# Performance work log

Hardware: AMD Instinct MI355X
Metric: run time of the kernel (lower is better)

## Reference

```python
import jax, jax.numpy as jnp
import numpy as np

N_NODES = 50000


def gcn_layer(x, src, dst, ew, W, b, n_nodes):
    # PyG GCNConv: add self-loops (weight 1), symmetric deg^-1/2 normalization,
    # linear transform, scatter-add aggregation at destination, then bias.
    loop = jnp.arange(n_nodes, dtype=src.dtype)
    s = jnp.concatenate([src, loop])
    d = jnp.concatenate([dst, loop])
    w = jnp.concatenate([ew, jnp.ones((n_nodes,), dtype=ew.dtype)])
    deg = jax.ops.segment_sum(w, d, num_segments=n_nodes)  # [N]
    dinv = jnp.where(deg > 0, jax.lax.rsqrt(jnp.where(deg > 0, deg, 1.0)), 0.0)
    norm = dinv[s] * w * dinv[d]  # [E+N]
    h = x @ W  # [N, out]
    msg = h[s] * norm[:, None]  # gather + scale, [E+N, out]
    out = jax.ops.segment_sum(msg, d, num_segments=n_nodes)  # scatter-add
    return out + b


def setup_inputs() -> dict:
    key = jax.random.key(0)
    k1, k2, k3, k4, k5, k6, k7 = jax.random.split(key, 7)
    N, E, C_IN, C_OUT = N_NODES, 600000, 128, 128
    x = jax.random.normal(k1, (N, C_IN), dtype=jnp.float32)
    edge_index = jax.random.randint(k2, (2, E), 0, N, dtype=jnp.int64)
    edge_weight = jax.random.uniform(k3, (E,), dtype=jnp.float32)
    # Glorot-style init like PyG's Linear default
    s1 = 1.0 / np.sqrt(C_IN)
    s2 = 1.0 / np.sqrt(C_OUT)
    W1 = jax.random.uniform(k4, (C_IN, C_OUT), jnp.float32, -s1, s1)
    b1 = jnp.zeros((C_OUT,), dtype=jnp.float32)
    W2 = jax.random.uniform(k5, (C_OUT, C_OUT), jnp.float32, -s2, s2)
    b2 = jnp.zeros((C_OUT,), dtype=jnp.float32)
    return {"x": x, "edge_index": edge_index, "edge_weight": edge_weight,
            "W1": W1, "b1": b1, "W2": W2, "b2": b2}


def reference(x, edge_index, edge_weight, W1, b1, W2, b2):
    src, dst = edge_index[0], edge_index[1]
    h = jax.nn.relu(gcn_layer(x, src, dst, edge_weight, W1, b1, N_NODES))
    return jax.nn.relu(gcn_layer(h, src, dst, edge_weight, W2, b2, N_NODES))
```

## Files before the change

### kernel.cpp

```cpp
#include <hip/hip_runtime.h>
#include <math.h>

#define CH   128
#define CH4  32
#define TPB  256
#define SCANB 1024
#define WIMG 16384
#define NREP 8
#define FIXS 1048576.0f

typedef __attribute__((ext_vector_type(8))) short short8;
typedef __attribute__((ext_vector_type(4))) float floatx4;
typedef __attribute__((ext_vector_type(8))) float float8;
typedef unsigned long long u64;

static __device__ __forceinline__ unsigned short f2bf(float f) {
    unsigned u = __float_as_uint(f);
    return (unsigned short)((u + 0x7fffu + ((u >> 16) & 1u)) >> 16);
}
static __device__ __forceinline__ float bf2f(unsigned short s) {
    return __uint_as_float(((unsigned)s) << 16);
}
static __device__ __forceinline__ float8 bf8_to_f8(short8 u) {
    float8 f;
    #pragma unroll
    for (int i = 0; i < 8; ++i) f[i] = bf2f((unsigned short)u[i]);
    return f;
}

__global__ void k_prep(const float* __restrict__ W1, const float* __restrict__ W2,
                       short* __restrict__ Wsplit, float4* __restrict__ zbase,
                       int nzero4, int nbPrep) {
    int bx = blockIdx.x;
    if (bx >= nbPrep) {
        int i = (bx - nbPrep) * TPB + threadIdx.x;
        if (i < nzero4) zbase[i] = make_float4(0.f, 0.f, 0.f, 0.f);
        return;
    }
    int i = bx * TPB + threadIdx.x;
    if (i >= 2 * CH * CH) return;
    int layer = i >> 14;
    int idx   = i & 16383;
    int k = idx >> 7, c = idx & 127;
    float w = (layer ? W2 : W1)[k * CH + c];
    unsigned short hi = f2bf(w);
    unsigned short lo = f2bf(w - bf2f(hi));
    int colh = c >> 6, nn = c & 63;
    int kt = k >> 5, q = (k & 31) >> 3, j = k & 7;
    int ns = nn >> 4, ln = q * 16 + (nn & 15);
    size_t base = (size_t)(layer * 2 + colh) * WIMG;
    size_t off  = ((size_t)(kt * 4 + ns) * 64 + ln) * 8 + j;
    Wsplit[base + off]        = (short)hi;
    Wsplit[base + 8192 + off] = (short)lo;
}

static __device__ __forceinline__ void gemm_body_f32(
        const float* __restrict__ X, const short* __restrict__ Wfrag,
        unsigned short* __restrict__ H, int n, int tile, int colh, int tid) {
    __shared__ __align__(16) short sW[2][4][4][64][8];
    {
        const float4* gsrc = (const float4*)Wfrag;
        float4* ldst = (float4*)sW;
        #pragma unroll
        for (int i = 0; i < 8; ++i)
            ldst[i * TPB + tid] = gsrc[i * TPB + tid];
    }
    __syncthreads();

    const int lane = tid & 63;
    const int wv   = tid >> 6;
    const int q    = lane >> 4;
    const int m    = lane & 15;
    const int row0 = tile * 64 + wv * 16;
    if (row0 >= n) return;

    int rrow = row0 + m;
    if (rrow > n - 1) rrow = n - 1;

    const float4* xr = (const float4*)(X + (size_t)rrow * CH);
    float4 xa[4][2];
    #pragma unroll
    for (int kt = 0; kt < 4; ++kt) {
        xa[kt][0] = xr[kt * 8 + q * 2 + 0];
        xa[kt][1] = xr[kt * 8 + q * 2 + 1];
    }

    floatx4 acc[4];
    #pragma unroll
    for (int ns = 0; ns < 4; ++ns) acc[ns] = (floatx4){0.f, 0.f, 0.f, 0.f};

    #pragma unroll
    for (int kt = 0; kt < 4; ++kt) {
        float xf[8] = { xa[kt][0].x, xa[kt][0].y, xa[kt][0].z, xa[kt][0].w,
                        xa[kt][1].x, xa[kt][1].y, xa[kt][1].z, xa[kt][1].w };
        short8 ah, al;
        #pragma unroll
        for (int j = 0; j < 8; ++j) {
            float v = xf[j];
            unsigned short h = f2bf(v);
            ah[j] = (short)h;
            al[j] = (short)f2bf(v - bf2f(h));
        }
        #pragma unroll
        for (int ns = 0; ns < 4; ++ns) {
            short8 bh = *(const short8*)&sW[0][kt][ns][lane][0];
            short8 bl = *(const short8*)&sW[1][kt][ns][lane][0];
            acc[ns] = __builtin_amdgcn_mfma_f32_16x16x32_bf16(ah, bh, acc[ns], 0, 0, 0);
            acc[ns] = __builtin_amdgcn_mfma_f32_16x16x32_bf16(al, bh, acc[ns], 0, 0, 0);
            acc[ns] = __builtin_amdgcn_mfma_f32_16x16x32_bf16(ah, bl, acc[ns], 0, 0, 0);
        }
    }

    #pragma unroll
    for (int ns = 0; ns < 4; ++ns) {
        #pragma unroll
        for (int reg = 0; reg < 4; ++reg) {
            int r = row0 + q * 4 + reg;
            if (r < n)
                H[(size_t)r * CH + colh * 64 + ns * 16 + m] = f2bf(acc[ns][reg]);
        }
    }
}

__global__ __launch_bounds__(TPB, 4)
void k_gemm_rank(const float* __restrict__ X, const short* __restrict__ Wsplit,
                 unsigned short* __restrict__ H, int n,
                 const int* __restrict__ dst, const float* __restrict__ ew,
                 u64* __restrict__ counts_rep, int E, int nbE4, int Np) {
    int bx = blockIdx.x;
    if (bx < nbE4) {
        int stride = nbE4 * TPB;
        int e = bx * TPB + threadIdx.x;
        #pragma unroll
        for (int it = 0; it < 4; ++it, e += stride) {
            if (e < E) {
                int d = dst[e];
                if ((unsigned)d < (unsigned)n) {
                    int rep = e & (NREP - 1);
                    u64 pk = (1ull << 40) |
                             (u64)(unsigned)__float2uint_rn(ew[e] * FIXS);
                    atomicAdd(&counts_rep[(size_t)rep * Np + d], pk);
                }
            }
        }
    } else {
        bx -= nbE4;
        int colh = bx & 1;
        gemm_body_f32(X, Wsplit + (size_t)colh * WIMG, H, n, bx >> 1, colh,
                      threadIdx.x);
    }
}

__global__ __launch_bounds__(SCANB)
void k_scan1(const u64* __restrict__ counts_rep, int Np,
             int* __restrict__ counts_tot, int* __restrict__ repoff8,
             int* __restrict__ row_start, float* __restrict__ dinv,
             int* __restrict__ partials, int* __restrict__ pp_s,
             int* __restrict__ done, int nb, int n) {
    __shared__ int swt[SCANB / 64];
    __shared__ int slastS;
    const int tid  = threadIdx.x;
    const int lane = tid & 63;
    const int wid  = tid >> 6;
    const int gid  = blockIdx.x * SCANB + tid;

    int c[NREP];
    int v = 0;
    u64 wsum = 0;
    #pragma unroll
    for (int r = 0; r < NREP; ++r) {
        u64 pk = (gid < n) ? counts_rep[(size_t)r * Np + gid] : 0ull;
        c[r] = (int)(pk >> 40);
        wsum += pk & ((1ull << 40) - 1);
        v += c[r];
    }
    int inc = v;
    #pragma unroll
    for (int off = 1; off < 64; off <<= 1) {
        int t = __shfl_up(inc, off, 64);
        if (lane >= off) inc += t;
    }
    if (lane == 63) swt[wid] = inc;
    __syncthreads();
    if (wid == 0) {
        int wv_ = (lane < SCANB / 64) ? swt[lane] : 0;
        int winc = wv_;
        #pragma unroll
        for (int off = 1; off < SCANB / 64; off <<= 1) {
            int t = __shfl_up(winc, off, 64);
            if (lane >= off) winc += t;
        }
        if (lane < SCANB / 64) swt[lane] = winc - wv_;
    }
    __syncthreads();
    const int myincl = inc + swt[wid];

    if (gid < n) {
        row_start[gid]  = myincl - v;
        counts_tot[gid] = v;
        dinv[gid] = rsqrtf(1.0f + (float)wsum * (1.0f / FIXS));
        int pre = 0;
        int ro[NREP];
        #pragma unroll
        for (int r = 0; r < NREP; ++r) { ro[r] = pre; pre += c[r]; }
        ((int4*)repoff8)[gid * 2 + 0] = make_int4(ro[0], ro[1], ro[2], ro[3]);
        ((int4*)repoff8)[gid * 2 + 1] = make_int4(ro[4], ro[5], ro[6], ro[7]);
    }
    if (tid == SCANB - 1) {
        partials[blockIdx.x] = myincl;
        __threadfence();
        int old = atomicAdd(done, 1);
        slastS = (old == nb - 1);
    }
    __syncthreads();
    if (slastS && tid < 64) {
        int pv = (tid < nb) ? atomicAdd(&partials[tid], 0) : 0;
        int i2 = pv;
        #pragma unroll
        for (int off = 1; off < 64; off <<= 1) {
            int t = __shfl_up(i2, off, 64);
            if ((tid & 63) >= off) i2 += t;
        }
        if (tid < nb) pp_s[tid] = i2 - pv;
    }
}

__global__ void k_fill(const int* __restrict__ src, const int* __restrict__ dst,
                       const float* __restrict__ ew, const int* __restrict__ row_start,
                       const int* __restrict__ pp_s, const int* __restrict__ repoff8,
                       u64* __restrict__ counts_rep, const float* __restrict__ dinv,
                       int2* __restrict__ edges, int E, int n, int Np) {
    int e = blockIdx.x * blockDim.x + threadIdx.x;
    if (e >= E) return;
    int s = src[e], d = dst[e];
    if ((unsigned)s >= (unsigned)n || (unsigned)d >= (unsigned)n) return;
    int rep = e & (NREP - 1);
    u64 old = atomicAdd(&counts_rep[(size_t)rep * Np + d], 0ull - (1ull << 40));
    int slot = (int)(old >> 40) - 1;
    int base = row_start[d] + pp_s[d >> 10] + repoff8[d * NREP + rep];
    edges[base + slot] = make_int2(s, __float_as_int(ew[e] * dinv[s]));
}

static __device__ __forceinline__ float8 agg_node8(
        const short8* __restrict__ h8, const int2* __restrict__ edges,
        float di, const float8 b, int node, int tx,
        const int* __restrict__ row_start, const int* __restrict__ pp_s,
        const int* __restrict__ counts) {
    float8 hv = bf8_to_f8(h8[(size_t)node * 16 + tx]);
    float8 acc;
    #pragma unroll
    for (int i = 0; i < 8; ++i) acc[i] = 0.f;

    int j   = row_start[node] + pp_s[node >> 10];
    int end = j + counts[node];

    for (; j + 8 <= end; j += 8) {
        int2 e[8];
        #pragma unroll
        for (int i = 0; i < 8; ++i) e[i] = edges[j + i];
        short8 g[8];
        #pragma unroll
        for (int i = 0; i < 8; ++i) g[i] = h8[(size_t)e[i].x * 16 + tx];
        #pragma unroll
        for (int i = 0; i < 8; ++i) {
            float w = __int_as_float(e[i].y);
            float8 gf = bf8_to_f8(g[i]);
            #pragma unroll
            for (int c = 0; c < 8; ++c) acc[c] += gf[c] * w;
        }
    }
    if (j + 4 <= end) {
        int2 e[4];
        #pragma unroll
        for (int i = 0; i < 4; ++i) e[i] = edges[j + i];
        short8 g[4];
        #pragma unroll
        for (int i = 0; i < 4; ++i) g[i] = h8[(size_t)e[i].x * 16 + tx];
        #pragma unroll
        for (int i = 0; i < 4; ++i) {
            float w = __int_as_float(e[i].y);
            float8 gf = bf8_to_f8(g[i]);
            #pragma unroll
            for (int c = 0; c < 8; ++c) acc[c] += gf[c] * w;
        }
        j += 4;
    }
    for (; j < end; ++j) {
        int2 e0 = edges[j];
        float w0 = __int_as_float(e0.y);
        float8 gf = bf8_to_f8(h8[(size_t)e0.x * 16 + tx]);
        #pragma unroll
        for (int c = 0; c < 8; ++c) acc[c] += gf[c] * w0;
    }

    float di2 = di * di;
    float8 o;
    #pragma unroll
    for (int c = 0; c < 8; ++c) o[c] = di2 * hv[c] + di * acc[c] + b[c];
    return o;
}

__global__ __launch_bounds__(TPB)
void k_agg_gemm(const unsigned short* __restrict__ h,
                const int* __restrict__ row_start, const int* __restrict__ pp_s,
                const int* __restrict__ counts, const int2* __restrict__ edges,
                const float* __restrict__ dinv, const float* __restrict__ bias,
                const short* __restrict__ W2img,
                unsigned short* __restrict__ h2, int n) {
    __shared__ __align__(16) short8 tile[16 * 17];
    const int tid = threadIdx.x;

    const int bnode0 = (int)blockIdx.x * 16;
    const int tx = tid & 15;
    const int tg = tid >> 4;
    const int node = bnode0 + tg;
    float8 b;
    #pragma unroll
    for (int c = 0; c < 8; ++c) b[c] = bias[tx * 8 + c];
    short8 u;
    if (node < n) {
        float8 o = agg_node8((const short8*)h, edges, dinv[node], b, node,
                             tx, row_start, pp_s, counts);
        #pragma unroll
        for (int c = 0; c < 8; ++c) u[c] = (short)f2bf(fmaxf(o[c], 0.f));
    } else {
        #pragma unroll
        for (int c = 0; c < 8; ++c) u[c] = 0;
    }
    tile[tg * 17 + tx] = u;
    __syncthreads();

    const int lane = tid & 63;
    const int wv   = tid >> 6;
    const int q    = lane >> 4;
    const int m    = lane & 15;
    const int ch   = wv & 1;
    const int ns0  = (wv >> 1) * 2;

    short8 a[4];
    #pragma unroll
    for (int kt = 0; kt < 4; ++kt)
        a[kt] = tile[m * 17 + kt * 4 + q];

    const short8* w2f = (const short8*)(W2img + (size_t)ch * WIMG);

    floatx4 acc[2];
    #pragma unroll
    for (int i = 0; i < 2; ++i) acc[i] = (floatx4){0.f, 0.f, 0.f, 0.f};

    #pragma unroll
    for (int kt = 0; kt < 4; ++kt) {
        #pragma unroll
        for (int i = 0; i < 2; ++i) {
            short8 bh = w2f[(kt * 4 + ns0 + i) * 64 + lane];
            acc[i] = __builtin_amdgcn_mfma_f32_16x16x32_bf16(a[kt], bh, acc[i],
                                                             0, 0, 0);
        }
    }

    #pragma unroll
    for (int i = 0; i < 2; ++i)
        #pragma unroll
        for (int reg = 0; reg < 4; ++reg) {
            int r = bnode0 + q * 4 + reg;
            if (r < n)
                h2[(size_t)r * CH + ch * 64 + (ns0 + i) * 16 + m] =
                    f2bf(acc[i][reg]);
        }
}

__global__ __launch_bounds__(TPB)
void k_aggregate2(const unsigned short* __restrict__ h,
                  const int* __restrict__ row_start, const int* __restrict__ pp_s,
                  const int* __restrict__ counts, const int2* __restrict__ edges,
                  const float* __restrict__ dinv, const float* __restrict__ bias,
                  float* __restrict__ out, int n) {
    int t = blockIdx.x * blockDim.x + threadIdx.x;
    int node = t >> 4;
    if (node >= n) return;
    int tx = t & 15;
    float8 b;
    #pragma unroll
    for (int c = 0; c < 8; ++c) b[c] = bias[tx * 8 + c];
    float8 o = agg_node8((const short8*)h, edges, dinv[node], b, node, tx,
                         row_start, pp_s, counts);
    float4 lo = make_float4(fmaxf(o[0], 0.f), fmaxf(o[1], 0.f),
                            fmaxf(o[2], 0.f), fmaxf(o[3], 0.f));
    float4 hi = make_float4(fmaxf(o[4], 0.f), fmaxf(o[5], 0.f),
                            fmaxf(o[6], 0.f), fmaxf(o[7], 0.f));
    ((float4*)out)[(size_t)node * CH4 + tx * 2 + 0] = lo;
    ((float4*)out)[(size_t)node * CH4 + tx * 2 + 1] = hi;
}

extern "C" void kernel_launch(void* const* d_in, const int* in_sizes, int n_in,
                              void* d_out, int out_size, void* d_ws, size_t ws_size,
                              hipStream_t stream) {
    const float* x  = (const float*)d_in[0];
    const int*   ei = (const int*)d_in[1];
    const float* ew = (const float*)d_in[2];
    const float* W1 = (const float*)d_in[3];
    const float* b1 = (const float*)d_in[4];
    const float* W2 = (const float*)d_in[5];
    const float* b2 = (const float*)d_in[6];
    float* out = (float*)d_out;

    const int N = in_sizes[0] / CH;
    const int E = in_sizes[2];
    const int* src = ei;
    const int* dst = ei + E;

    size_t Np = ((size_t)N + 255) & ~(size_t)255;
    float* ws          = (float*)d_ws;
    float* dinv        = ws;
    unsigned short* h  = (unsigned short*)(dinv + Np);
    unsigned short* h2 = h + (size_t)N * CH;
    u64*   counts_rep  = (u64*)(h2 + (size_t)N * CH);
    int*   done        = (int*)(counts_rep + NREP * Np);
    int    nzero4      = (int)((2 * NREP * Np + 64) / 4);
    int*  counts_tot   = done + 64;
    int*  row_start    = counts_tot + Np;
    int*  repoff8      = row_start + Np;
    int*  partials     = repoff8 + NREP * Np;
    int*  pp_s         = partials + 64;
    int2* edges        = (int2*)(pp_s + 64);
    short* Wsplit      = (short*)(edges + E);

    const int nbE    = (E + TPB - 1) / TPB;
    const int nbE4   = (E + TPB * 4 - 1) / (TPB * 4);
    const int nbAgg  = (int)(((size_t)N * 16 + TPB - 1) / TPB);
    const int nbScan = (N + SCANB - 1) / SCANB;
    const int nbGemm = 2 * ((N + 63) / 64);
    const int nbAG   = (N + 15) / 16;
    const int nbPrep = (2 * CH * CH + TPB - 1) / TPB;
    const int nbZero = (nzero4 + TPB - 1) / TPB;

    k_prep     <<<nbPrep + nbZero, TPB, 0, stream>>>(W1, W2, Wsplit,
                                                     (float4*)counts_rep,
                                                     nzero4, nbPrep);

    k_gemm_rank<<<nbE4 + nbGemm, TPB, 0, stream>>>(x, Wsplit, h, N, dst, ew,
                                                   counts_rep, E, nbE4, (int)Np);
    k_scan1    <<<nbScan, SCANB, 0, stream>>>(counts_rep, (int)Np, counts_tot,
                                              repoff8, row_start, dinv,
                                              partials, pp_s, done, nbScan, N);
    k_fill     <<<nbE, TPB, 0, stream>>>(src, dst, ew, row_start, pp_s, repoff8,
                                         counts_rep, dinv, edges, E, N, (int)Np);

    k_agg_gemm <<<nbAG, TPB, 0, stream>>>(h, row_start, pp_s, counts_tot,
                                          edges, dinv, b1,
                                          Wsplit + 2 * (size_t)WIMG, h2, N);
    k_aggregate2<<<nbAgg, TPB, 0, stream>>>(h2, row_start, pp_s, counts_tot,
                                            edges, dinv, b2, out, N);
}
```

Before: 223.7 us.

## Record edge rank during counting and pad CSR rows to multiples of eight

The counting pass now saves each edge's slot from the atomic's return value, so the fill pass writes edges directly without a second atomic on the per-node counters. The scan pads every row length up to a multiple of eight, and extra fill blocks write zero-weight dummy edges (source 0) into the padding. The aggregation loop then runs only full 8-wide batches with no 4-wide or scalar tail. In exchange the code adds a rank array and more padded edge storage, and it gathers wasted dummy rows of node 0.

```diff
diff --git a/kernel.cpp b/kernel.cpp
--- a/kernel.cpp
+++ b/kernel.cpp
@@ -126,7 +126,8 @@
 void k_gemm_rank(const float* __restrict__ X, const short* __restrict__ Wsplit,
                  unsigned short* __restrict__ H, int n,
                  const int* __restrict__ dst, const float* __restrict__ ew,
-                 u64* __restrict__ counts_rep, int E, int nbE4, int Np) {
+                 u64* __restrict__ counts_rep, int* __restrict__ rank,
+                 int E, int nbE4, int Np) {
     int bx = blockIdx.x;
     if (bx < nbE4) {
         int stride = nbE4 * TPB;
@@ -139,7 +140,8 @@
                     int rep = e & (NREP - 1);
                     u64 pk = (1ull << 40) |
                              (u64)(unsigned)__float2uint_rn(ew[e] * FIXS);
-                    atomicAdd(&counts_rep[(size_t)rep * Np + d], pk);
+                    u64 old = atomicAdd(&counts_rep[(size_t)rep * Np + d], pk);
+                    rank[e] = (int)(old >> 40);
                 }
             }
         }
@@ -174,7 +176,8 @@
         wsum += pk & ((1ull << 40) - 1);
         v += c[r];
     }
-    int inc = v;
+    const int vp = (v + 7) & ~7;
+    int inc = vp;
     #pragma unroll
     for (int off = 1; off < 64; off <<= 1) {
         int t = __shfl_up(inc, off, 64);
@@ -196,7 +199,7 @@
     const int myincl = inc + swt[wid];
 
     if (gid < n) {
-        row_start[gid]  = myincl - v;
+        row_start[gid]  = myincl - vp;
         counts_tot[gid] = v;
         dinv[gid] = rsqrtf(1.0f + (float)wsum * (1.0f / FIXS));
         int pre = 0;
@@ -228,17 +231,28 @@
 __global__ void k_fill(const int* __restrict__ src, const int* __restrict__ dst,
                        const float* __restrict__ ew, const int* __restrict__ row_start,
                        const int* __restrict__ pp_s, const int* __restrict__ repoff8,
-                       u64* __restrict__ counts_rep, const float* __restrict__ dinv,
-                       int2* __restrict__ edges, int E, int n, int Np) {
-    int e = blockIdx.x * blockDim.x + threadIdx.x;
+                       const int* __restrict__ rank, const float* __restrict__ dinv,
+                       const int* __restrict__ counts_tot,
+                       int2* __restrict__ edges, int E, int n, int nbE) {
+    int bx = blockIdx.x;
+    if (bx >= nbE) {
+        int node = (bx - nbE) * TPB + threadIdx.x;
+        if (node >= n) return;
+        int v  = counts_tot[node];
+        int vp = (v + 7) & ~7;
+        if (v == vp) return;
+        int base = row_start[node] + pp_s[node >> 10] + v;
+        for (int k = 0; k < vp - v; ++k)
+            edges[base + k] = make_int2(0, 0);
+        return;
+    }
+    int e = bx * TPB + threadIdx.x;
     if (e >= E) return;
     int s = src[e], d = dst[e];
     if ((unsigned)s >= (unsigned)n || (unsigned)d >= (unsigned)n) return;
     int rep = e & (NREP - 1);
-    u64 old = atomicAdd(&counts_rep[(size_t)rep * Np + d], 0ull - (1ull << 40));
-    int slot = (int)(old >> 40) - 1;
     int base = row_start[d] + pp_s[d >> 10] + repoff8[d * NREP + rep];
-    edges[base + slot] = make_int2(s, __float_as_int(ew[e] * dinv[s]));
+    edges[base + rank[e]] = make_int2(s, __float_as_int(ew[e] * dinv[s]));
 }
 
 static __device__ __forceinline__ float8 agg_node8(
@@ -252,9 +266,9 @@
     for (int i = 0; i < 8; ++i) acc[i] = 0.f;
 
     int j   = row_start[node] + pp_s[node >> 10];
-    int end = j + counts[node];
-
-    for (; j + 8 <= end; j += 8) {
+    int end = j + ((counts[node] + 7) & ~7);
+
+    for (; j < end; j += 8) {
         int2 e[8];
         #pragma unroll
         for (int i = 0; i < 8; ++i) e[i] = edges[j + i];
@@ -268,29 +282,6 @@
             #pragma unroll
             for (int c = 0; c < 8; ++c) acc[c] += gf[c] * w;
         }
-    }
-    if (j + 4 <= end) {
-        int2 e[4];
-        #pragma unroll
-        for (int i = 0; i < 4; ++i) e[i] = edges[j + i];
-        short8 g[4];
-        #pragma unroll
-        for (int i = 0; i < 4; ++i) g[i] = h8[(size_t)e[i].x * 16 + tx];
-        #pragma unroll
-        for (int i = 0; i < 4; ++i) {
-            float w = __int_as_float(e[i].y);
-            float8 gf = bf8_to_f8(g[i]);
-            #pragma unroll
-            for (int c = 0; c < 8; ++c) acc[c] += gf[c] * w;
-        }
-        j += 4;
-    }
-    for (; j < end; ++j) {
-        int2 e0 = edges[j];
-        float w0 = __int_as_float(e0.y);
-        float8 gf = bf8_to_f8(h8[(size_t)e0.x * 16 + tx]);
-        #pragma unroll
-        for (int c = 0; c < 8; ++c) acc[c] += gf[c] * w0;
     }
 
     float di2 = di * di;
@@ -409,7 +400,9 @@
     const int* src = ei;
     const int* dst = ei + E;
 
-    size_t Np = ((size_t)N + 255) & ~(size_t)255;
+    size_t Np   = ((size_t)N + 255) & ~(size_t)255;
+    size_t Ep   = ((size_t)E + 63) & ~(size_t)63;
+    size_t Epad = (size_t)E + 8 * Np;
     float* ws          = (float*)d_ws;
     float* dinv        = ws;
     unsigned short* h  = (unsigned short*)(dinv + Np);
@@ -420,12 +413,14 @@
     int*  counts_tot   = done + 64;
     int*  row_start    = counts_tot + Np;
     int*  repoff8      = row_start + Np;
-    int*  partials     = repoff8 + NREP * Np;
+    int*  rank         = repoff8 + NREP * Np;
+    int*  partials     = rank + Ep;
     int*  pp_s         = partials + 64;
     int2* edges        = (int2*)(pp_s + 64);
-    short* Wsplit      = (short*)(edges + E);
+    short* Wsplit      = (short*)(edges + Epad);
 
     const int nbE    = (E + TPB - 1) / TPB;
+    const int nbN    = (N + TPB - 1) / TPB;
     const int nbE4   = (E + TPB * 4 - 1) / (TPB * 4);
     const int nbAgg  = (int)(((size_t)N * 16 + TPB - 1) / TPB);
     const int nbScan = (N + SCANB - 1) / SCANB;
@@ -439,12 +434,14 @@
                                                      nzero4, nbPrep);
 
     k_gemm_rank<<<nbE4 + nbGemm, TPB, 0, stream>>>(x, Wsplit, h, N, dst, ew,
-                                                   counts_rep, E, nbE4, (int)Np);
+                                                   counts_rep, rank, E, nbE4,
+                                                   (int)Np);
     k_scan1    <<<nbScan, SCANB, 0, stream>>>(counts_rep, (int)Np, counts_tot,
                                               repoff8, row_start, dinv,
                                               partials, pp_s, done, nbScan, N);
-    k_fill     <<<nbE, TPB, 0, stream>>>(src, dst, ew, row_start, pp_s, repoff8,
-                                         counts_rep, dinv, edges, E, N, (int)Np);
+    k_fill     <<<nbE + nbN, TPB, 0, stream>>>(src, dst, ew, row_start, pp_s,
+                                               repoff8, rank, dinv, counts_tot,
+                                               edges, E, N, nbE);
 
     k_agg_gemm <<<nbAG, TPB, 0, stream>>>(h, row_start, pp_s, counts_tot,
                                           edges, dinv, b1,
```

Result: faster. 199.5 us (-10.8%).
